# Performance work log

Measured on AMD Instinct MI355X. Metric: run time of the kernel, lower is better.

## Reference

```python
import jax, jax.numpy as jnp
import numpy as np


def setup_inputs() -> dict:
    key = jax.random.key(0)
    k1, k2 = jax.random.split(key)
    bz, c, h, w = 8, 512, 64, 64
    x = jax.random.normal(k1, (bz, c, h, w), dtype=jnp.float32)
    # binary mask over spatial positions; flag is its flattened view (must be consistent)
    mask = jax.random.randint(k2, (h, w), 0, 2, dtype=jnp.int32)
    flag = mask.reshape(-1)
    return {"input": x, "mask": mask, "flag": flag,
            "shift_sz": 1, "stride": 1, "triple_w": 1}


def reference(input, mask, flag, shift_sz, stride, triple_w):
    # input: [B, C, H, W]; former = first C/2 channels (decoder feats),
    # latter = last C/2 channels (encoder feats). shift_sz=stride=1 -> 1x1 patches,
    # i.e. per-pixel feature vectors.
    bz, c, h, w = input.shape
    ch = c // 2
    S = h * w
    former = input[:, :ch]                      # [B, ch, H, W]
    latter = input[:, ch:]                      # [B, ch, H, W]

    f = former.reshape(bz, ch, S).transpose(0, 2, 1)   # [B, S, ch] query pixels
    l = latter.reshape(bz, ch, S).transpose(0, 2, 1)   # [B, S, ch] key pixels

    # _norm: L2-normalize latter patches (rows)
    l_norm = l / jnp.maximum(jnp.linalg.norm(l, axis=-1, keepdims=True), 1e-12)

    # cosine-style similarity between every former pixel and every latter pixel
    sim = jnp.einsum('bqc,bkc->bqk', f, l_norm)        # [B, S, S]

    # only non-masked (flag==0) latter pixels are valid match candidates
    neg = jnp.asarray(-1e30, sim.dtype)
    sim = jnp.where((flag == 0)[None, None, :], sim, neg)
    idx = jnp.argmax(sim, axis=-1)                     # [B, S] nearest-neighbor index

    # gather matched latter pixels; paste only at masked (flag==1) positions,
    # zero elsewhere (masked_fill_(inv_ex_mask, 0) zeroes the non-mask region)
    shifted = jnp.take_along_axis(l, idx[..., None], axis=1)       # [B, S, ch]
    shifted = jnp.where((flag == 1)[None, :, None], shifted, 0.0)
    shifted = shifted.transpose(0, 2, 1).reshape(bz, ch, h, w)

    return jnp.concatenate([former, latter, shifted], axis=1)       # [B, 3*ch, H, W]
```

## Files before the change

### kernel.cpp

```cpp
#include <hip/hip_runtime.h>

#define S    4096
#define CH   256
#define NB   8

#define BM   128
#define BN   64
#define KSPLIT 8

#define SFF  256.0f
#define SLL  1024.0f

#define NEG_INF (-3.402823466e38f)

typedef _Float16 half8 __attribute__((ext_vector_type(8)));
typedef float    f32x4 __attribute__((ext_vector_type(4)));

__global__ void compact(const int* __restrict__ flag, int* __restrict__ cnts,
                        int* __restrict__ qlist, int* __restrict__ klist,
                        int* __restrict__ qpos,  int* __restrict__ kpos) {
    __shared__ int sq[256], sk[256];
    int t = threadIdx.x;
    int base = t * 16;
    int f[16];
    int nq = 0, nk = 0;
    #pragma unroll
    for (int i = 0; i < 16; ++i) {
        f[i] = flag[base + i];
        nq += (f[i] == 1);
        nk += (f[i] == 0);
    }
    sq[t] = nq; sk[t] = nk;
    __syncthreads();
    for (int off = 1; off < 256; off <<= 1) {
        int vq = sq[t], vk = sk[t];
        int aq = (t >= off) ? sq[t - off] : 0;
        int ak = (t >= off) ? sk[t - off] : 0;
        __syncthreads();
        sq[t] = vq + aq; sk[t] = vk + ak;
        __syncthreads();
    }
    int pq = sq[t] - nq;
    int pk = sk[t] - nk;
    #pragma unroll
    for (int i = 0; i < 16; ++i) {
        if (f[i] == 1) { qpos[base + i] = pq; qlist[pq++] = base + i; }
        else           { kpos[base + i] = pk; klist[pk++] = base + i; }
    }
    if (t == 255) { cnts[0] = sq[255]; cnts[1] = sk[255]; }
}

__global__ void invnorm_k(const float* __restrict__ x, float* __restrict__ invn) {
    int k4 = blockIdx.x * 256 + threadIdx.x;
    int b  = blockIdx.y;
    const float4* base = (const float4*)(x + ((size_t)b * 512 + 256) * S) + k4;
    float4 acc = { 0.f, 0.f, 0.f, 0.f };
    #pragma unroll 8
    for (int c = 0; c < CH; ++c) {
        float4 v = base[(size_t)c * (S / 4)];
        acc.x += v.x * v.x; acc.y += v.y * v.y;
        acc.z += v.z * v.z; acc.w += v.w * v.w;
    }
    float4 r;
    r.x = 1.0f / fmaxf(sqrtf(acc.x), 1e-12f);
    r.y = 1.0f / fmaxf(sqrtf(acc.y), 1e-12f);
    r.z = 1.0f / fmaxf(sqrtf(acc.z), 1e-12f);
    r.w = 1.0f / fmaxf(sqrtf(acc.w), 1e-12f);
    ((float4*)(invn + ((size_t)b << 12)))[k4] = r;
}

__global__ void pack_both(const float* __restrict__ x, const int* __restrict__ flag,
                          const int* __restrict__ qpos, const int* __restrict__ kpos,
                          const float* __restrict__ invn, float* __restrict__ out) {
    __shared__ float T[16][257];
    const int b    = blockIdx.z;
    const int t    = threadIdx.x;
    const int s    = blockIdx.x * 256 + t;
    const bool isF = (blockIdx.y < 4);
    const int c0b  = (isF ? blockIdx.y : (blockIdx.y - 4)) * 64;

    _Float16* H;
    const float* src;
    bool active;
    int row;
    float w;
    if (isF) {
        H      = (_Float16*)(out + (size_t)b * 768 * S);
        src    = x + (size_t)b * 512 * S + blockIdx.x * 256;
        active = (flag[s] == 1);
        row    = active ? qpos[s] : 0;
        w      = SFF;
    } else {
        H      = (_Float16*)(out + (size_t)b * 768 * S) + 2 * (size_t)S * CH;
        src    = x + ((size_t)b * 512 + 256) * S + blockIdx.x * 256;
        active = (flag[s] == 0);
        row    = active ? kpos[s] : 0;
        w      = active ? invn[((size_t)b << 12) + s] * SLL : 0.f;
    }
    _Float16* L = H + (size_t)S * CH;

    for (int c0 = c0b; c0 < c0b + 64; c0 += 16) {
        #pragma unroll
        for (int i = 0; i < 16; ++i)
            T[i][t] = src[(size_t)(c0 + i) * S + t];
        __syncthreads();
        if (active) {
            #pragma unroll
            for (int g = 0; g < 2; ++g) {
                union { _Float16 u[8]; float4 v; } hb, lb;
                #pragma unroll
                for (int j = 0; j < 8; ++j) {
                    float v = T[g * 8 + j][t] * w;
                    _Float16 h = (_Float16)v;
                    hb.u[j] = h;
                    lb.u[j] = (_Float16)(v - (float)h);
                }
                *(float4*)&H[(size_t)row * CH + c0 + g * 8] = hb.v;
                *(float4*)&L[(size_t)row * CH + c0 + g * 8] = lb.v;
            }
        }
        __syncthreads();
    }
}

__global__ void zero_pad(const int* __restrict__ cnts, float* __restrict__ out) {
    const int b  = blockIdx.y;
    const int Aq = cnts[0], Ak = cnts[1];
    const int aqp = (Aq + BM - 1) & ~(BM - 1);
    const int akp = (Ak + BN - 1) & ~(BN - 1);
    _Float16* pb = (_Float16*)(out + (size_t)b * 768 * S);
    int i = blockIdx.x * 256 + threadIdx.x;
    half8 z = { 0, 0, 0, 0, 0, 0, 0, 0 };
    if (i < 8192) {
        int panel = i >> 12, idx = i & 4095;
        int row = Aq + (idx >> 5);
        if (row < aqp)
            *(half8*)(pb + (size_t)panel * S * CH + (size_t)row * CH + (idx & 31) * 8) = z;
    } else {
        int j = i - 8192, panel = j >> 11, jdx = j & 2047;
        int row = Ak + (jdx >> 5);
        if (row < akp)
            *(half8*)(pb + (size_t)(2 + panel) * S * CH + (size_t)row * CH + (jdx & 31) * 8) = z;
    }
}

#define MFMA(A, B, C) __builtin_amdgcn_mfma_f32_16x16x32_f16((A), (B), (C), 0, 0, 0)

#define GLDS(SRC, OFF) __builtin_amdgcn_global_load_lds( \
    (const __attribute__((address_space(1))) void*)(SRC), \
    (__attribute__((address_space(3))) void*)(lds + (OFF)), 16, 0, 0)

#define STAGE(OFF) do { GLDS(s4, (OFF) + woff); GLDS(s5, (OFF) + 4096 + woff); } while (0)

#define ADV() do { \
    if (tn + 1 < nchunk) { \
        if ((tn & 7) == 7) { s4 += 32320; s5 += 32320; } \
        else               { s4 += 64;    s5 += 64;    } \
    } \
    ++tn; \
} while (0)

#define FOLD() do { \
    _Pragma("unroll") \
    for (int nt = 0; nt < 4; ++nt) { \
        int kp = kpb + nt * 16; \
        if (kp < Ak) { \
            _Pragma("unroll") \
            for (int mt = 0; mt < 2; ++mt) { \
                _Pragma("unroll") \
                for (int r = 0; r < 4; ++r) { \
                    const int ix = mt * 4 + r; \
                    float sv = acc[mt][nt][r]; \
                    if (sv > rm[ix]) { rm[ix] = sv; ri[ix] = kp; } \
                } \
            } \
        } \
        acc[0][nt] = (f32x4){0.f, 0.f, 0.f, 0.f}; \
        acc[1][nt] = (f32x4){0.f, 0.f, 0.f, 0.f}; \
    } \
    kpb += 64; \
} while (0)

#define CBODY(BASE, CC) do { \
    const char* _bb = lds + (BASE); \
    half8 bh0 = *(const half8*)(_bb + boff_h[0]); \
    half8 bl0 = *(const half8*)(_bb + boff_l[0]); \
    half8 bh1 = *(const half8*)(_bb + boff_h[1]); \
    half8 bl1 = *(const half8*)(_bb + boff_l[1]); \
    half8 bh2 = *(const half8*)(_bb + boff_h[2]); \
    half8 bl2 = *(const half8*)(_bb + boff_l[2]); \
    half8 bh3 = *(const half8*)(_bb + boff_h[3]); \
    half8 bl3 = *(const half8*)(_bb + boff_l[3]); \
    acc[0][0] = MFMA(ah0[CC], bh0, acc[0][0]); \
    acc[1][0] = MFMA(ah1[CC], bh0, acc[1][0]); \
    acc[0][0] = MFMA(ah0[CC], bl0, acc[0][0]); \
    acc[1][0] = MFMA(ah1[CC], bl0, acc[1][0]); \
    acc[0][0] = MFMA(al0[CC], bh0, acc[0][0]); \
    acc[1][0] = MFMA(al1[CC], bh0, acc[1][0]); \
    acc[0][1] = MFMA(ah0[CC], bh1, acc[0][1]); \
    acc[1][1] = MFMA(ah1[CC], bh1, acc[1][1]); \
    acc[0][1] = MFMA(ah0[CC], bl1, acc[0][1]); \
    acc[1][1] = MFMA(ah1[CC], bl1, acc[1][1]); \
    acc[0][1] = MFMA(al0[CC], bh1, acc[0][1]); \
    acc[1][1] = MFMA(al1[CC], bh1, acc[1][1]); \
    acc[0][2] = MFMA(ah0[CC], bh2, acc[0][2]); \
    acc[1][2] = MFMA(ah1[CC], bh2, acc[1][2]); \
    acc[0][2] = MFMA(ah0[CC], bl2, acc[0][2]); \
    acc[1][2] = MFMA(ah1[CC], bl2, acc[1][2]); \
    acc[0][2] = MFMA(al0[CC], bh2, acc[0][2]); \
    acc[1][2] = MFMA(al1[CC], bh2, acc[1][2]); \
    acc[0][3] = MFMA(ah0[CC], bh3, acc[0][3]); \
    acc[1][3] = MFMA(ah1[CC], bh3, acc[1][3]); \
    acc[0][3] = MFMA(ah0[CC], bl3, acc[0][3]); \
    acc[1][3] = MFMA(ah1[CC], bl3, acc[1][3]); \
    acc[0][3] = MFMA(al0[CC], bh3, acc[0][3]); \
    acc[1][3] = MFMA(al1[CC], bh3, acc[1][3]); \
} while (0)

#define PHASE(J) do { \
    asm volatile("s_waitcnt vmcnt(4)" ::: "memory"); \
    __builtin_amdgcn_s_barrier(); \
    STAGE(sto); ADV(); \
    STAGE(sto + 8192); ADV(); \
    __builtin_amdgcn_s_setprio(1); \
    CBODY(rdo,        2 * (J)); \
    CBODY(rdo + 8192, 2 * (J) + 1); \
    __builtin_amdgcn_s_setprio(0); \
    rdo = (rdo == 32768) ? 0 : rdo + 16384; \
    sto = (sto == 32768) ? 0 : sto + 16384; \
} while (0)

__launch_bounds__(256)
__global__ void argmax_mfma(const float* __restrict__ outbuf,
                            const int*  __restrict__ cnts,
                            float* __restrict__ pmax,
                            int*   __restrict__ pidx) {
    __shared__ __align__(1024) char lds[6 * 8192];

    const int Aq    = cnts[0];
    const int Ak    = cnts[1];
    const int b     = blockIdx.y;
    const int split = blockIdx.x & (KSPLIT - 1);
    const int q0    = (blockIdx.x >> 3) * BM;
    if (q0 >= Aq) return;

    const int tid  = threadIdx.x;
    const int lane = tid & 63;
    const int wid  = tid >> 6;
    const int l15  = lane & 15;
    const int l4   = lane >> 4;
    const int woff = wid * 1024;

    const _Float16* pb  = (const _Float16*)(outbuf + (size_t)b * 768 * S);
    const _Float16* FHg = pb;
    const _Float16* FLg = pb + (size_t)S * CH;
    const _Float16* LHg = pb + 2 * (size_t)S * CH;
    const _Float16* LLg = pb + 3 * (size_t)S * CH;

    const int nkt = (Ak + BN - 1) / BN;
    const int kt0 = (nkt * split) / KSPLIT;
    const int kt1 = (nkt * (split + 1)) / KSPLIT;
    const int nchunk = (kt1 - kt0) * 8;

    float rm[8]; int ri[8];
    #pragma unroll
    for (int i = 0; i < 8; ++i) { rm[i] = NEG_INF; ri[i] = 0; }

    int boff_h[4], boff_l[4];
    #pragma unroll
    for (int nt = 0; nt < 4; ++nt) {
        int rowb = nt * 16 + l15;
        int swzb = (rowb & 7) << 4;
        boff_h[nt] = rowb * 128 + ((l4 * 16)        ^ swzb);
        boff_l[nt] = rowb * 128 + (((l4 * 16) + 64) ^ swzb);
    }

    if (nchunk > 0) {
        half8 ah0[8], al0[8], ah1[8], al1[8];
        {
            const size_t ro0 = (size_t)(q0 + wid * 32 + l15)      * CH + l4 * 8;
            const size_t ro1 = (size_t)(q0 + wid * 32 + 16 + l15) * CH + l4 * 8;
            #pragma unroll
            for (int cc = 0; cc < 8; ++cc) {
                ah0[cc] = *(const half8*)(FHg + ro0 + cc * 32);
                al0[cc] = *(const half8*)(FLg + ro0 + cc * 32);
                ah1[cc] = *(const half8*)(FHg + ro1 + cc * 32);
                al1[cc] = *(const half8*)(FLg + ro1 + cc * 32);
            }
        }

        const char *s4, *s5;
        {
            #define LSRC(P) ({ int s_ = (P) * 256 + tid; int row_ = s_ >> 3; \
                int ls_ = (s_ & 7) ^ (row_ & 7); \
                (const char*)(((ls_ < 4) ? LHg : LLg) + (size_t)(kt0 * BN + row_) * CH + (ls_ & 3) * 8); })
            s4 = LSRC(0); s5 = LSRC(1);
            #undef LSRC
        }
        int tn = 0;

        f32x4 acc[2][4];
        #pragma unroll
        for (int mt = 0; mt < 2; ++mt)
            #pragma unroll
            for (int nt = 0; nt < 4; ++nt) acc[mt][nt] = (f32x4){0.f, 0.f, 0.f, 0.f};

        int kpb = kt0 * BN + l15;

        STAGE(0);     ADV();
        STAGE(8192);  ADV();
        STAGE(16384); ADV();
        STAGE(24576); ADV();

        int rdo = 0;
        int sto = 32768;
        const int ngroup = kt1 - kt0;
        for (int g = 0; g < ngroup; ++g) {
            PHASE(0);
            PHASE(1);
            PHASE(2);
            PHASE(3);
            FOLD();
        }
    }

    #pragma unroll
    for (int mt = 0; mt < 2; ++mt) {
        #pragma unroll
        for (int r = 0; r < 4; ++r) {
            const int ix = mt * 4 + r;
            float m = rm[ix]; int id = ri[ix];
            #pragma unroll
            for (int off = 8; off; off >>= 1) {
                float om = __shfl_xor(m, off, 64);
                int   oi = __shfl_xor(id, off, 64);
                if (om > m || (om == m && oi < id)) { m = om; id = oi; }
            }
            if (l15 == 0) {
                int qp = q0 + wid * 32 + mt * 16 + l4 * 4 + r;
                if (qp < Aq) {
                    size_t o = ((size_t)((b << 12) + qp)) * KSPLIT + split;
                    pmax[o] = m;
                    pidx[o] = id;
                }
            }
        }
    }
}

__global__ void combine(const int* __restrict__ cnts, const int* __restrict__ qlist,
                        const int* __restrict__ klist,
                        const float* __restrict__ pmax, const int* __restrict__ pidx,
                        int* __restrict__ idxb) {
    int qp = blockIdx.x * 256 + threadIdx.x;
    int b  = blockIdx.y;
    if (qp >= cnts[0]) return;
    size_t base = (size_t)((b << 12) + qp) * KSPLIT;
    float m = pmax[base]; int id = pidx[base];
    #pragma unroll
    for (int s = 1; s < KSPLIT; ++s) {
        float om = pmax[base + s]; int oi = pidx[base + s];
        if (om > m) { m = om; id = oi; }
    }
    idxb[((size_t)b << 12) + qlist[qp]] = klist[id];
}

__global__ void writeback(const float* __restrict__ x, const int* __restrict__ flag,
                          const int* __restrict__ idxb, float* __restrict__ out) {
    int i = blockIdx.x * 256 + threadIdx.x;
    int b = blockIdx.y;
    int c = i >> 10;
    float4* dst = (float4*)(out + (size_t)b * 768 * S) + i;
    if (c < 512) {
        *dst = ((const float4*)(x + (size_t)b * 512 * S))[i];
    } else {
        const float* src = x + ((size_t)b * 512 + 256 + (c - 512)) * S;
        const int* ib = idxb + ((size_t)b << 12);
        int q = (i & 1023) * 4;
        float4 v = { 0.f, 0.f, 0.f, 0.f };
        if (flag[q + 0] == 1) v.x = src[ib[q + 0]];
        if (flag[q + 1] == 1) v.y = src[ib[q + 1]];
        if (flag[q + 2] == 1) v.z = src[ib[q + 2]];
        if (flag[q + 3] == 1) v.w = src[ib[q + 3]];
        *dst = v;
    }
}

extern "C" void kernel_launch(void* const* d_in, const int* in_sizes, int n_in,
                              void* d_out, int out_size, void* d_ws, size_t ws_size,
                              hipStream_t stream) {
    const float* x    = (const float*)d_in[0];
    const int*   flag = (const int*)d_in[2];
    float*       out  = (float*)d_out;

    char* ws = (char*)d_ws;
    int*   cnts  = (int*)(ws);
    int*   qlist = (int*)(ws + 1024);
    int*   klist = (int*)(ws + 17408);
    int*   qpos  = (int*)(ws + 33792);
    int*   kpos  = (int*)(ws + 50176);
    float* invn  = (float*)(ws + 66560);
    int*   idxb  = (int*)(ws + 197632);
    float* pmax  = (float*)(ws + 328704);
    int*   pidx  = (int*)(ws + 1377280);

    hipLaunchKernelGGL(compact,     dim3(1),                     dim3(256), 0, stream, flag, cnts, qlist, klist, qpos, kpos);
    hipLaunchKernelGGL(invnorm_k,   dim3(S / 4 / 256, NB),       dim3(256), 0, stream, x, invn);
    hipLaunchKernelGGL(pack_both,   dim3(S / 256, 8, NB),        dim3(256), 0, stream, x, flag, qpos, kpos, invn, out);
    hipLaunchKernelGGL(zero_pad,    dim3(48, NB),                dim3(256), 0, stream, cnts, out);
    hipLaunchKernelGGL(argmax_mfma, dim3((S / BM) * KSPLIT, NB), dim3(256), 0, stream, out, cnts, pmax, pidx);
    hipLaunchKernelGGL(combine,     dim3(S / 256, NB),           dim3(256), 0, stream, cnts, qlist, klist, pmax, pidx, idxb);
    hipLaunchKernelGGL(writeback,   dim3(768 * 1024 / 256, NB),  dim3(256), 0, stream, x, flag, idxb, out);
}
```

Measured before the change: 176.4 us.

## Fuse inverse-norm into pack kernel and tile former panels for MFMA loads

Removes the separate invnorm kernel. Each latter-pack block now reads all 256 channels twice: once to compute its own L2 norm and once to scale and split into fp16 hi/lo. Former hi/lo panels are stored in a 16-row tiled layout, so the argmax kernel's A-fragment loads become contiguous per lane group. The fused path trades a kernel launch and the invn round trip for more work per latter block and a lower grid count for the latter half (one block per spatial tile instead of four).

```diff
diff --git a/kernel.cpp b/kernel.cpp
--- a/kernel.cpp
+++ b/kernel.cpp
@@ -50,76 +50,91 @@
     if (t == 255) { cnts[0] = sq[255]; cnts[1] = sk[255]; }
 }
 
-__global__ void invnorm_k(const float* __restrict__ x, float* __restrict__ invn) {
-    int k4 = blockIdx.x * 256 + threadIdx.x;
-    int b  = blockIdx.y;
-    const float4* base = (const float4*)(x + ((size_t)b * 512 + 256) * S) + k4;
-    float4 acc = { 0.f, 0.f, 0.f, 0.f };
-    #pragma unroll 8
-    for (int c = 0; c < CH; ++c) {
-        float4 v = base[(size_t)c * (S / 4)];
-        acc.x += v.x * v.x; acc.y += v.y * v.y;
-        acc.z += v.z * v.z; acc.w += v.w * v.w;
-    }
-    float4 r;
-    r.x = 1.0f / fmaxf(sqrtf(acc.x), 1e-12f);
-    r.y = 1.0f / fmaxf(sqrtf(acc.y), 1e-12f);
-    r.z = 1.0f / fmaxf(sqrtf(acc.z), 1e-12f);
-    r.w = 1.0f / fmaxf(sqrtf(acc.w), 1e-12f);
-    ((float4*)(invn + ((size_t)b << 12)))[k4] = r;
-}
-
 __global__ void pack_both(const float* __restrict__ x, const int* __restrict__ flag,
                           const int* __restrict__ qpos, const int* __restrict__ kpos,
-                          const float* __restrict__ invn, float* __restrict__ out) {
+                          float* __restrict__ out) {
     __shared__ float T[16][257];
-    const int b    = blockIdx.z;
-    const int t    = threadIdx.x;
-    const int s    = blockIdx.x * 256 + t;
-    const bool isF = (blockIdx.y < 4);
-    const int c0b  = (isF ? blockIdx.y : (blockIdx.y - 4)) * 64;
-
-    _Float16* H;
-    const float* src;
-    bool active;
-    int row;
-    float w;
-    if (isF) {
-        H      = (_Float16*)(out + (size_t)b * 768 * S);
-        src    = x + (size_t)b * 512 * S + blockIdx.x * 256;
-        active = (flag[s] == 1);
-        row    = active ? qpos[s] : 0;
-        w      = SFF;
+    const int b = blockIdx.z;
+    const int t = threadIdx.x;
+    const int s = blockIdx.x * 256 + t;
+
+    if (blockIdx.y < 4) {
+        const int c0b = blockIdx.y * 64;
+        const float* src = x + (size_t)b * 512 * S + blockIdx.x * 256;
+        const bool active = (flag[s] == 1);
+        const int row = active ? qpos[s] : 0;
+        half8* F2 = (half8*)(out + (size_t)b * 768 * S);
+        const int g  = row >> 4;
+        const int sr = row & 15;
+        for (int c0 = c0b; c0 < c0b + 64; c0 += 16) {
+            #pragma unroll
+            for (int i = 0; i < 16; ++i)
+                T[i][t] = src[(size_t)(c0 + i) * S + t];
+            __syncthreads();
+            if (active) {
+                #pragma unroll
+                for (int g8 = 0; g8 < 2; ++g8) {
+                    const int c  = c0 + g8 * 8;
+                    const int cc = c >> 5;
+                    const int l4 = (c >> 3) & 3;
+                    half8 hb, lb;
+                    #pragma unroll
+                    for (int j = 0; j < 8; ++j) {
+                        float v = T[g8 * 8 + j][t] * SFF;
+                        _Float16 h = (_Float16)v;
+                        hb[j] = h;
+                        lb[j] = (_Float16)(v - (float)h);
+                    }
+                    F2[(size_t)(((g * 2 + 0) * 8 + cc) * 64) + sr * 4 + l4] = hb;
+                    F2[(size_t)(((g * 2 + 1) * 8 + cc) * 64) + sr * 4 + l4] = lb;
+                }
+            }
+            __syncthreads();
+        }
     } else {
-        H      = (_Float16*)(out + (size_t)b * 768 * S) + 2 * (size_t)S * CH;
-        src    = x + ((size_t)b * 512 + 256) * S + blockIdx.x * 256;
-        active = (flag[s] == 0);
-        row    = active ? kpos[s] : 0;
-        w      = active ? invn[((size_t)b << 12) + s] * SLL : 0.f;
-    }
-    _Float16* L = H + (size_t)S * CH;
-
-    for (int c0 = c0b; c0 < c0b + 64; c0 += 16) {
-        #pragma unroll
-        for (int i = 0; i < 16; ++i)
-            T[i][t] = src[(size_t)(c0 + i) * S + t];
-        __syncthreads();
-        if (active) {
-            #pragma unroll
-            for (int g = 0; g < 2; ++g) {
-                union { _Float16 u[8]; float4 v; } hb, lb;
+        const float* src = x + ((size_t)b * 512 + 256) * S + blockIdx.x * 256;
+        const bool active = (flag[s] == 0);
+        const int row = active ? kpos[s] : 0;
+        _Float16* LH = (_Float16*)(out + (size_t)b * 768 * S) + 2 * (size_t)S * CH;
+        _Float16* LL = LH + (size_t)S * CH;
+
+        float acc = 0.f;
+        for (int c0 = 0; c0 < CH; c0 += 16) {
+            #pragma unroll
+            for (int i = 0; i < 16; ++i)
+                T[i][t] = src[(size_t)(c0 + i) * S + t];
+            __syncthreads();
+            #pragma unroll
+            for (int i = 0; i < 16; ++i) {
+                float v = T[i][t];
+                acc += v * v;
+            }
+            __syncthreads();
+        }
+        const float w = active ? (1.0f / fmaxf(sqrtf(acc), 1e-12f)) * SLL : 0.f;
+
+        for (int c0 = 0; c0 < CH; c0 += 16) {
+            #pragma unroll
+            for (int i = 0; i < 16; ++i)
+                T[i][t] = src[(size_t)(c0 + i) * S + t];
+            __syncthreads();
+            if (active) {
                 #pragma unroll
-                for (int j = 0; j < 8; ++j) {
-                    float v = T[g * 8 + j][t] * w;
-                    _Float16 h = (_Float16)v;
-                    hb.u[j] = h;
-                    lb.u[j] = (_Float16)(v - (float)h);
+                for (int g8 = 0; g8 < 2; ++g8) {
+                    union { _Float16 u[8]; float4 v; } hb, lb;
+                    #pragma unroll
+                    for (int j = 0; j < 8; ++j) {
+                        float v = T[g8 * 8 + j][t] * w;
+                        _Float16 h = (_Float16)v;
+                        hb.u[j] = h;
+                        lb.u[j] = (_Float16)(v - (float)h);
+                    }
+                    *(float4*)&LH[(size_t)row * CH + c0 + g8 * 8] = hb.v;
+                    *(float4*)&LL[(size_t)row * CH + c0 + g8 * 8] = lb.v;
                 }
-                *(float4*)&H[(size_t)row * CH + c0 + g * 8] = hb.v;
-                *(float4*)&L[(size_t)row * CH + c0 + g * 8] = lb.v;
-            }
-        }
-        __syncthreads();
+            }
+            __syncthreads();
+        }
     }
 }
 
@@ -132,10 +147,13 @@
     int i = blockIdx.x * 256 + threadIdx.x;
     half8 z = { 0, 0, 0, 0, 0, 0, 0, 0 };
     if (i < 8192) {
-        int panel = i >> 12, idx = i & 4095;
-        int row = Aq + (idx >> 5);
-        if (row < aqp)
-            *(half8*)(pb + (size_t)panel * S * CH + (size_t)row * CH + (idx & 31) * 8) = z;
+        int p = i >> 12, rem = i & 4095;
+        int row = Aq + (rem >> 5);
+        int sl  = rem & 31;
+        if (row < aqp) {
+            half8* F2 = (half8*)pb;
+            F2[(size_t)((((row >> 4) * 2 + p) * 8 + (sl >> 2)) * 64) + (row & 15) * 4 + (sl & 3)] = z;
+        }
     } else {
         int j = i - 8192, panel = j >> 11, jdx = j & 2047;
         int row = Ak + (jdx >> 5);
@@ -252,8 +270,6 @@
     const int woff = wid * 1024;
 
     const _Float16* pb  = (const _Float16*)(outbuf + (size_t)b * 768 * S);
-    const _Float16* FHg = pb;
-    const _Float16* FLg = pb + (size_t)S * CH;
     const _Float16* LHg = pb + 2 * (size_t)S * CH;
     const _Float16* LLg = pb + 3 * (size_t)S * CH;
 
@@ -278,14 +294,15 @@
     if (nchunk > 0) {
         half8 ah0[8], al0[8], ah1[8], al1[8];
         {
-            const size_t ro0 = (size_t)(q0 + wid * 32 + l15)      * CH + l4 * 8;
-            const size_t ro1 = (size_t)(q0 + wid * 32 + 16 + l15) * CH + l4 * 8;
+            const half8* F2 = (const half8*)pb;
+            const int g0 = (q0 >> 4) + wid * 2;
+            const int lo = l15 * 4 + l4;
             #pragma unroll
             for (int cc = 0; cc < 8; ++cc) {
-                ah0[cc] = *(const half8*)(FHg + ro0 + cc * 32);
-                al0[cc] = *(const half8*)(FLg + ro0 + cc * 32);
-                ah1[cc] = *(const half8*)(FHg + ro1 + cc * 32);
-                al1[cc] = *(const half8*)(FLg + ro1 + cc * 32);
+                ah0[cc] = F2[(size_t)((((g0    ) * 2 + 0) * 8 + cc) * 64) + lo];
+                al0[cc] = F2[(size_t)((((g0    ) * 2 + 1) * 8 + cc) * 64) + lo];
+                ah1[cc] = F2[(size_t)((((g0 + 1) * 2 + 0) * 8 + cc) * 64) + lo];
+                al1[cc] = F2[(size_t)((((g0 + 1) * 2 + 1) * 8 + cc) * 64) + lo];
             }
         }
 
@@ -399,14 +416,12 @@
     int*   klist = (int*)(ws + 17408);
     int*   qpos  = (int*)(ws + 33792);
     int*   kpos  = (int*)(ws + 50176);
-    float* invn  = (float*)(ws + 66560);
-    int*   idxb  = (int*)(ws + 197632);
-    float* pmax  = (float*)(ws + 328704);
-    int*   pidx  = (int*)(ws + 1377280);
+    int*   idxb  = (int*)(ws + 66560);
+    float* pmax  = (float*)(ws + 197632);
+    int*   pidx  = (int*)(ws + 1246208);
 
     hipLaunchKernelGGL(compact,     dim3(1),                     dim3(256), 0, stream, flag, cnts, qlist, klist, qpos, kpos);
-    hipLaunchKernelGGL(invnorm_k,   dim3(S / 4 / 256, NB),       dim3(256), 0, stream, x, invn);
-    hipLaunchKernelGGL(pack_both,   dim3(S / 256, 8, NB),        dim3(256), 0, stream, x, flag, qpos, kpos, invn, out);
+    hipLaunchKernelGGL(pack_both,   dim3(S / 256, 5, NB),        dim3(256), 0, stream, x, flag, qpos, kpos, out);
     hipLaunchKernelGGL(zero_pad,    dim3(48, NB),                dim3(256), 0, stream, cnts, out);
     hipLaunchKernelGGL(argmax_mfma, dim3((S / BM) * KSPLIT, NB), dim3(256), 0, stream, out, cnts, pmax, pidx);
     hipLaunchKernelGGL(combine,     dim3(S / 256, NB),           dim3(256), 0, stream, cnts, qlist, klist, pmax, pidx, idxb);
```

Result: faster. 163.1 us (-7.5%).
